# Kernel tuning notes

Measured on AMD Instinct MI355X. Metric: run time of the kernel, lower is better.

Reference implementation:

```python
import jax, jax.numpy as jnp
import numpy as np

B, T, C, H = 2, 2048, 1024, 16
D = C // H  # head_dim = 64

def setup_inputs() -> dict:
    key = jax.random.key(0)
    k1, k2, k3, k4, k5 = jax.random.split(key, 5)
    x = jax.random.normal(k1, (B, T, C), dtype=jnp.float32)
    # RoPE tables (realistic frequencies)
    inv_freq = 1.0 / (10000.0 ** (jnp.arange(0, D // 2, dtype=jnp.float32) / (D // 2)))
    pos = jnp.arange(T, dtype=jnp.float32)
    ang = pos[:, None] * inv_freq[None, :]          # (T, D/2)
    cos, sin = jnp.cos(ang), jnp.sin(ang)
    # causal mask (True = keep)
    mask = jnp.tril(jnp.ones((T, T), dtype=bool))
    W_qkv = jax.random.normal(k2, (3 * C, C), dtype=jnp.float32) * (1.0 / np.sqrt(C))
    W_out = jax.random.normal(k3, (C, C), dtype=jnp.float32) * (1.0 / np.sqrt(C))
    return {"x": x, "cos": cos, "sin": sin, "mask": mask, "W_qkv": W_qkv, "W_out": W_out}

def apply_rope(x, cos, sin):
    # x: (B, H, T, D); cos/sin: (T, D/2)
    d = x.shape[-1] // 2
    x1, x2 = x[..., :d], x[..., d:]
    c = cos[None, None, :x.shape[2], :]
    s = sin[None, None, :x.shape[2], :]
    return jnp.concatenate([x1 * c - x2 * s, x2 * c + x1 * s], axis=-1)

def reference(x, cos, sin, mask, W_qkv, W_out):
    b, t, c = x.shape
    qkv = (x @ W_qkv.T).reshape(b, t, 3, H, D)
    q, k, v = qkv[:, :, 0], qkv[:, :, 1], qkv[:, :, 2]   # (b, t, H, D)
    q = q.transpose(0, 2, 1, 3)
    k = k.transpose(0, 2, 1, 3)
    v = v.transpose(0, 2, 1, 3)                           # (b, H, t, D)
    q = apply_rope(q, cos, sin)
    k = apply_rope(k, cos, sin)
    attn = jnp.einsum('bhqd,bhkd->bhqk', q, k) / jnp.sqrt(jnp.asarray(D, x.dtype))
    attn = jnp.where(mask[None, None, :, :], attn, -jnp.inf)
    attn = jax.nn.softmax(attn, axis=-1)
    out = jnp.einsum('bhqk,bhkd->bhqd', attn, v)          # (b, H, t, D)
    out = out.transpose(0, 2, 1, 3).reshape(b, t, c)
    return out @ W_out.T
```

## Files before the change

kernel.cpp:

```cpp
#include <hip/hip_runtime.h>
#include <stdint.h>

typedef __bf16 bf16;
typedef __bf16 bf16x4 __attribute__((ext_vector_type(4)));
typedef __bf16 bf16x8 __attribute__((ext_vector_type(8)));
typedef float f32x4 __attribute__((ext_vector_type(4)));

#define TSEQ 2048
#define NHEAD 16
#define HDIM 64
#define CDIM 1024

#define AS1(p) ((const __attribute__((address_space(1))) void*)(p))
#define AS3(p) ((__attribute__((address_space(3))) void*)(p))

#if __has_builtin(__builtin_amdgcn_exp2f)
#define EXP2(x) __builtin_amdgcn_exp2f(x)
#else
#define EXP2(x) exp2f(x)
#endif

__global__ __launch_bounds__(256) void cast3_bf16(const float* __restrict__ in1, int n1,
                                                  const float* __restrict__ in2, int n2,
                                                  const float* __restrict__ in3, int n3,
                                                  bf16* __restrict__ out1,
                                                  bf16* __restrict__ out2,
                                                  bf16* __restrict__ out3) {
  int i = (blockIdx.x * 256 + threadIdx.x) * 8;
  const float* src;
  bf16* dst;
  if (i < n1) {
    src = in1 + i; dst = out1 + i;
  } else if (i < n1 + n2) {
    src = in2 + (i - n1); dst = out2 + (i - n1);
  } else if (i < n1 + n2 + n3) {
    src = in3 + (i - n1 - n2); dst = out3 + (i - n1 - n2);
  } else {
    return;
  }
  float4 a = *(const float4*)src;
  float4 b = *(const float4*)(src + 4);
  bf16x8 r;
  r[0] = (bf16)a.x; r[1] = (bf16)a.y; r[2] = (bf16)a.z; r[3] = (bf16)a.w;
  r[4] = (bf16)b.x; r[5] = (bf16)b.y; r[6] = (bf16)b.z; r[7] = (bf16)b.w;
  *(bf16x8*)dst = r;
}

__global__ __launch_bounds__(256) void gemm_qkv_rope(const bf16* __restrict__ A,
                                                     const bf16* __restrict__ B,
                                                     const float* __restrict__ cosb,
                                                     const float* __restrict__ sinb,
                                                     bf16* __restrict__ Qb,
                                                     bf16* __restrict__ Kb,
                                                     bf16* __restrict__ Vt) {
  constexpr int K = 1024;
  __shared__ bf16 smem[8704];
  const int t = threadIdx.x;
  const int w = t >> 6, l = t & 63, g = l >> 4, ln = l & 15;
  const int wm = (w >> 1) * 64, wn = (w & 1) * 64;
  const int m0 = blockIdx.x * 128, n0 = blockIdx.y * 128;
  const int r0 = t >> 2, kc0 = (t & 3) * 8;

  f32x4 acc[4][4] = {};

  for (int k0 = 0; k0 < K; k0 += 32) {
    __syncthreads();
    __builtin_amdgcn_global_load_lds(AS1(A + (size_t)(m0 + r0) * K + k0 + kc0),
                                     AS3(&smem[t * 8]), 16, 0, 0);
    __builtin_amdgcn_global_load_lds(AS1(A + (size_t)(m0 + r0 + 64) * K + k0 + kc0),
                                     AS3(&smem[(t + 256) * 8]), 16, 0, 0);
    __builtin_amdgcn_global_load_lds(AS1(B + (size_t)(n0 + r0) * K + k0 + kc0),
                                     AS3(&smem[4096 + t * 8]), 16, 0, 0);
    __builtin_amdgcn_global_load_lds(AS1(B + (size_t)(n0 + r0 + 64) * K + k0 + kc0),
                                     AS3(&smem[4096 + (t + 256) * 8]), 16, 0, 0);
    __syncthreads();
    bf16x8 af[4], bfr[4];
#pragma unroll
    for (int i = 0; i < 4; i++) {
      af[i] = *(const bf16x8*)&smem[(wm + i * 16 + ln) * 32 + g * 8];
      bfr[i] = *(const bf16x8*)&smem[4096 + (wn + i * 16 + ln) * 32 + g * 8];
    }
#pragma unroll
    for (int i = 0; i < 4; i++)
#pragma unroll
      for (int j = 0; j < 4; j++)
        acc[i][j] = __builtin_amdgcn_mfma_f32_16x16x32_bf16(af[i], bfr[j], acc[i][j], 0, 0, 0);
  }

  const int part = n0 >> 10;
  if (part < 2) {
    bf16* dst = part ? Kb : Qb;
    const float qs = part ? 1.0f : 0.18033688011112042f;
#pragma unroll
    for (int i = 0; i < 4; i++)
#pragma unroll
      for (int j = 0; j < 2; j++) {
        int nl = (n0 & 1023) + wn + j * 16 + ln;
        int h = nl >> 6, d = nl & 31;
#pragma unroll
        for (int r = 0; r < 4; r++) {
          int row = m0 + wm + i * 16 + g * 4 + r;
          int tok = row & (TSEQ - 1), bb = row >> 11;
          float c = cosb[tok * 32 + d], s = sinb[tok * 32 + d];
          float a1 = acc[i][j][r], a2 = acc[i][j + 2][r];
          size_t ob = ((size_t)(bb * NHEAD + h) * TSEQ + tok) * HDIM + d;
          dst[ob] = (bf16)((a1 * c - a2 * s) * qs);
          dst[ob + 32] = (bf16)((a2 * c + a1 * s) * qs);
        }
      }
  } else {
    const int bb = m0 >> 11;
    const int tbase = m0 & (TSEQ - 1);
    const int nbase = n0 - 2048;
#pragma unroll
    for (int pass = 0; pass < 2; pass++) {
      __syncthreads();
      if ((w >> 1) == pass) {
#pragma unroll
        for (int i = 0; i < 4; i++)
#pragma unroll
          for (int j = 0; j < 4; j++) {
            int lr = i * 16 + g * 4;
            int lc = wn + j * 16 + ln;
#pragma unroll
            for (int r = 0; r < 4; r++)
              smem[(lr + r) * 132 + lc] = (bf16)acc[i][j][r];
          }
      }
      __syncthreads();
      for (int c = t; c < 1024; c += 256) {
        int ch = c >> 3, tc = c & 7;
        bf16x8 o;
#pragma unroll
        for (int j2 = 0; j2 < 8; j2++) o[j2] = smem[(tc * 8 + j2) * 132 + ch];
        int n = nbase + ch;
        int h = n >> 6, d = n & 63;
        *(bf16x8*)(Vt + ((size_t)((bb * NHEAD + h) * HDIM + d)) * TSEQ +
                   tbase + pass * 64 + tc * 8) = o;
      }
    }
  }
}

__global__ __launch_bounds__(256) void gemm_out(const bf16* __restrict__ A,
                                                const bf16* __restrict__ B,
                                                float* __restrict__ C,
                                                int M, int N, int K) {
  __shared__ bf16 smem[8192];
  const int t = threadIdx.x;
  const int w = t >> 6, l = t & 63, g = l >> 4, ln = l & 15;
  const int wm = (w >> 1) * 64, wn = (w & 1) * 64;
  const int m0 = blockIdx.x * 128, n0 = blockIdx.y * 128;
  const int r0 = t >> 2, kc0 = (t & 3) * 8;

  f32x4 acc[4][4] = {};

  for (int k0 = 0; k0 < K; k0 += 32) {
    __syncthreads();
    __builtin_amdgcn_global_load_lds(AS1(A + (size_t)(m0 + r0) * K + k0 + kc0),
                                     AS3(&smem[t * 8]), 16, 0, 0);
    __builtin_amdgcn_global_load_lds(AS1(A + (size_t)(m0 + r0 + 64) * K + k0 + kc0),
                                     AS3(&smem[(t + 256) * 8]), 16, 0, 0);
    __builtin_amdgcn_global_load_lds(AS1(B + (size_t)(n0 + r0) * K + k0 + kc0),
                                     AS3(&smem[4096 + t * 8]), 16, 0, 0);
    __builtin_amdgcn_global_load_lds(AS1(B + (size_t)(n0 + r0 + 64) * K + k0 + kc0),
                                     AS3(&smem[4096 + (t + 256) * 8]), 16, 0, 0);
    __syncthreads();
    bf16x8 af[4], bfr[4];
#pragma unroll
    for (int i = 0; i < 4; i++) {
      af[i] = *(const bf16x8*)&smem[(wm + i * 16 + ln) * 32 + g * 8];
      bfr[i] = *(const bf16x8*)&smem[4096 + (wn + i * 16 + ln) * 32 + g * 8];
    }
#pragma unroll
    for (int i = 0; i < 4; i++)
#pragma unroll
      for (int j = 0; j < 4; j++)
        acc[i][j] = __builtin_amdgcn_mfma_f32_16x16x32_bf16(af[i], bfr[j], acc[i][j], 0, 0, 0);
  }
#pragma unroll
  for (int i = 0; i < 4; i++)
#pragma unroll
    for (int j = 0; j < 4; j++) {
      int row = m0 + wm + i * 16 + g * 4;
      int col = n0 + wn + j * 16 + ln;
#pragma unroll
      for (int r = 0; r < 4; r++)
        C[(size_t)(row + r) * N + col] = acc[i][j][r];
    }
}

__global__ __launch_bounds__(1024, 4) void attn_fwd(const bf16* __restrict__ Q,
                                                    const bf16* __restrict__ K,
                                                    const bf16* __restrict__ Vt,
                                                    bf16* __restrict__ ctx) {
  __shared__ __align__(16) char smem_raw[65536];
  bf16* Ks = (bf16*)smem_raw;
  bf16* VTs = (bf16*)(smem_raw + 16384);
  bf16* Ps = (bf16*)(smem_raw + 32768);
  float* Mbuf = (float*)smem_raw;
  float* Lbuf = (float*)(smem_raw + 32768);

  const int t = threadIdx.x;
  const int w = t >> 6;
  const int p = w >> 3;
  const int wq = w & 7;
  const int l = t & 63, g = l >> 4, ln = l & 15;
  const int bid = blockIdx.x;
  const int bh = bid & 31;
  const int qb0 = 15 - (bid >> 5);
  const size_t base = (size_t)bh * TSEQ * HDIM;

  const int q0 = qb0 * 128;
  const int qwb = q0 + wq * 16;
  const int dtile = qwb >> 6;
  const int q_g = qwb + ln;
  const int lswz = (ln & 7) * 8;

  const int ts = t >> 9;
  const int tt = t & 511;
  const int r0 = tt >> 3, ch0 = (tt & 7) * 8;
  const int sidx = r0 * 64 + (((tt & 7) ^ (r0 & 7)) * 8);

  bf16x8 bq[2];
  bq[0] = *(const bf16x8*)(Q + base + (size_t)q_g * HDIM + g * 8);
  bq[1] = *(const bf16x8*)(Q + base + (size_t)q_g * HDIM + 32 + g * 8);

  const bf16* kp = K + base + (size_t)(ts * 64 + r0) * HDIM + ch0;
  const bf16* vp = Vt + base + (size_t)r0 * TSEQ + ts * 64 + ch0;
  bf16x8 kr = *(const bf16x8*)kp;
  bf16x8 vr = *(const bf16x8*)vp;

  f32x4 acc[4] = {};
  float l_run = 0.f;

  for (int i = 0; i <= qb0; i++) {
    __syncthreads();
    *(bf16x8*)&Ks[ts * 4096 + sidx] = kr;
    *(bf16x8*)&VTs[ts * 4096 + sidx] = vr;
    __syncthreads();
    if (i < qb0) {
      kr = *(const bf16x8*)(kp + (size_t)(i + 1) * 128 * HDIM);
      vr = *(const bf16x8*)(vp + (i + 1) * 128);
    }
    const int kt = 2 * i + p;
    if (kt <= dtile) {
      f32x4 st[4] = {};
      __builtin_amdgcn_s_setprio(1);
#pragma unroll
      for (int step = 0; step < 2; step++)
#pragma unroll
        for (int mt = 0; mt < 4; mt++) {
          bf16x8 ak = *(const bf16x8*)&Ks[p * 4096 + (mt * 16 + ln) * 64 +
                                          ((step * 32 + g * 8) ^ lswz)];
          st[mt] = __builtin_amdgcn_mfma_f32_16x16x32_bf16(ak, bq[step], st[mt], 0, 0, 0);
        }
      __builtin_amdgcn_s_setprio(0);
      float vals[16];
      if (kt == dtile) {
#pragma unroll
        for (int mt = 0; mt < 4; mt++)
#pragma unroll
          for (int r = 0; r < 4; r++) {
            int kg = kt * 64 + mt * 16 + g * 4 + r;
            vals[mt * 4 + r] = (kg <= q_g) ? st[mt][r] : -INFINITY;
          }
      } else {
#pragma unroll
        for (int mt = 0; mt < 4; mt++)
#pragma unroll
          for (int r = 0; r < 4; r++) vals[mt * 4 + r] = st[mt][r];
      }
      float psum = 0.f;
#pragma unroll
      for (int i2 = 0; i2 < 16; i2++) {
        float pv = EXP2(vals[i2]);
        vals[i2] = pv;
        psum += pv;
      }
      psum += __shfl_xor(psum, 16);
      psum += __shfl_xor(psum, 32);
      l_run += psum;
#pragma unroll
      for (int mt = 0; mt < 4; mt++) {
        bf16x4 pk;
#pragma unroll
        for (int r = 0; r < 4; r++) pk[r] = (bf16)vals[mt * 4 + r];
        *(bf16x4*)&Ps[w * 1024 + ln * 64 +
                      (((mt * 16 + (g >> 1) * 8) ^ lswz) + (g & 1) * 4)] = pk;
      }
      __builtin_amdgcn_s_setprio(1);
#pragma unroll
      for (int step = 0; step < 2; step++) {
        bf16x8 ap = *(const bf16x8*)&Ps[w * 1024 + ln * 64 + ((step * 32 + g * 8) ^ lswz)];
#pragma unroll
        for (int nt = 0; nt < 4; nt++) {
          bf16x8 bv = *(const bf16x8*)&VTs[p * 4096 + (nt * 16 + ln) * 64 +
                                           ((step * 32 + g * 8) ^ lswz)];
          acc[nt] = __builtin_amdgcn_mfma_f32_16x16x32_bf16(ap, bv, acc[nt], 0, 0, 0);
        }
      }
      __builtin_amdgcn_s_setprio(0);
    }
  }

  __syncthreads();
  if (p == 1) {
#pragma unroll
    for (int nt = 0; nt < 4; nt++)
      *(f32x4*)&Mbuf[(wq * 64 + l) * 16 + nt * 4] = acc[nt];
    Lbuf[wq * 64 + l] = l_run;
  }
  __syncthreads();
  if (p == 0) {
#pragma unroll
    for (int nt = 0; nt < 4; nt++) acc[nt] += *(const f32x4*)&Mbuf[(wq * 64 + l) * 16 + nt * 4];
    l_run += Lbuf[wq * 64 + l];
    float inv = 1.0f / l_run;
    float lrow[4];
#pragma unroll
    for (int r = 0; r < 4; r++) lrow[r] = __shfl(inv, g * 4 + r, 64);
    const int b = bh >> 4, h = bh & (NHEAD - 1);
#pragma unroll
    for (int nt = 0; nt < 4; nt++)
#pragma unroll
      for (int r = 0; r < 4; r++) {
        int q = qwb + g * 4 + r;
        ctx[(size_t)(b * TSEQ + q) * CDIM + h * HDIM + nt * 16 + ln] =
            (bf16)(acc[nt][r] * lrow[r]);
      }
  }
}

extern "C" void kernel_launch(void* const* d_in, const int* in_sizes, int n_in,
                              void* d_out, int out_size, void* d_ws, size_t ws_size,
                              hipStream_t stream) {
  const float* x = (const float*)d_in[0];
  const float* cosb = (const float*)d_in[1];
  const float* sinb = (const float*)d_in[2];
  const float* Wqkv = (const float*)d_in[4];
  const float* Wout = (const float*)d_in[5];
  float* out = (float*)d_out;

  char* ws = (char*)d_ws;
  bf16* x_bf = (bf16*)ws;
  bf16* ctx = (bf16*)ws;
  bf16* Wqkv_bf = (bf16*)(ws + 8388608);
  bf16* Wout_bf = (bf16*)(ws + 14680064);
  bf16* Qb = (bf16*)(ws + 16777216);
  bf16* Kb = (bf16*)(ws + 25165824);
  bf16* Vt = (bf16*)(ws + 33554432);

  cast3_bf16<<<(4194304 + 3145728 + 1048576) / 8 / 256, 256, 0, stream>>>(
      x, 4194304, Wqkv, 3145728, Wout, 1048576, x_bf, Wqkv_bf, Wout_bf);
  gemm_qkv_rope<<<dim3(32, 24), 256, 0, stream>>>(x_bf, Wqkv_bf, cosb, sinb, Qb, Kb, Vt);
  attn_fwd<<<512, 1024, 0, stream>>>(Qb, Kb, Vt, ctx);
  gemm_out<<<dim3(32, 8), 256, 0, stream>>>(ctx, Wout_bf, out, 4096, 1024, 1024);
}
```

Measured before the change: 184.3 us.

## Triple-buffer LDS in QKV GEMM with async global-to-LDS prefetch

```diff
diff --git a/kernel.cpp b/kernel.cpp
--- a/kernel.cpp
+++ b/kernel.cpp
@@ -54,7 +54,121 @@
                                                      bf16* __restrict__ Kb,
                                                      bf16* __restrict__ Vt) {
   constexpr int K = 1024;
-  __shared__ bf16 smem[8704];
+  __shared__ bf16 smem[24576];
+  const int t = threadIdx.x;
+  const int w = t >> 6, l = t & 63, g = l >> 4, ln = l & 15;
+  const int wm = (w >> 1) * 64, wn = (w & 1) * 64;
+  const int m0 = blockIdx.x * 128, n0 = blockIdx.y * 128;
+  const int r0 = t >> 2, kc0 = (t & 3) * 8;
+
+  f32x4 acc[4][4] = {};
+
+#define STAGE_G1(buf, k0)                                                             \
+  do {                                                                                \
+    __builtin_amdgcn_global_load_lds(AS1(A + (size_t)(m0 + r0) * K + (k0) + kc0),     \
+                                     AS3(&smem[(buf) * 8192 + t * 8]), 16, 0, 0);     \
+    __builtin_amdgcn_global_load_lds(AS1(A + (size_t)(m0 + r0 + 64) * K + (k0) + kc0),\
+                                     AS3(&smem[(buf) * 8192 + (t + 256) * 8]), 16, 0, 0); \
+    __builtin_amdgcn_global_load_lds(AS1(B + (size_t)(n0 + r0) * K + (k0) + kc0),     \
+                                     AS3(&smem[(buf) * 8192 + 4096 + t * 8]), 16, 0, 0);  \
+    __builtin_amdgcn_global_load_lds(AS1(B + (size_t)(n0 + r0 + 64) * K + (k0) + kc0),\
+                                     AS3(&smem[(buf) * 8192 + 4096 + (t + 256) * 8]), 16, 0, 0); \
+  } while (0)
+
+  STAGE_G1(0, 0);
+  STAGE_G1(1, 32);
+  asm volatile("s_waitcnt vmcnt(4) lgkmcnt(0)" ::: "memory");
+  __builtin_amdgcn_s_barrier();
+  asm volatile("" ::: "memory");
+
+  for (int it = 0; it < 32; ++it) {
+    const int cur = it % 3;
+    if (it < 30) STAGE_G1((it + 2) % 3, (it + 2) * 32);
+    const bf16* sa = &smem[cur * 8192];
+    const bf16* sb = &smem[cur * 8192 + 4096];
+    bf16x8 af[4], bfr[4];
+#pragma unroll
+    for (int i = 0; i < 4; i++) {
+      af[i] = *(const bf16x8*)&sa[(wm + i * 16 + ln) * 32 + g * 8];
+      bfr[i] = *(const bf16x8*)&sb[(wn + i * 16 + ln) * 32 + g * 8];
+    }
+#pragma unroll
+    for (int i = 0; i < 4; i++)
+#pragma unroll
+      for (int j = 0; j < 4; j++)
+        acc[i][j] = __builtin_amdgcn_mfma_f32_16x16x32_bf16(af[i], bfr[j], acc[i][j], 0, 0, 0);
+    if (it < 30) {
+      asm volatile("s_waitcnt vmcnt(4) lgkmcnt(0)" ::: "memory");
+      __builtin_amdgcn_s_barrier();
+      asm volatile("" ::: "memory");
+    } else if (it == 30) {
+      asm volatile("s_waitcnt vmcnt(0) lgkmcnt(0)" ::: "memory");
+      __builtin_amdgcn_s_barrier();
+      asm volatile("" ::: "memory");
+    }
+  }
+#undef STAGE_G1
+
+  const int part = n0 >> 10;
+  if (part < 2) {
+    bf16* dst = part ? Kb : Qb;
+    const float qs = part ? 1.0f : 0.18033688011112042f;
+#pragma unroll
+    for (int i = 0; i < 4; i++)
+#pragma unroll
+      for (int j = 0; j < 2; j++) {
+        int nl = (n0 & 1023) + wn + j * 16 + ln;
+        int h = nl >> 6, d = nl & 31;
+#pragma unroll
+        for (int r = 0; r < 4; r++) {
+          int row = m0 + wm + i * 16 + g * 4 + r;
+          int tok = row & (TSEQ - 1), bb = row >> 11;
+          float c = cosb[tok * 32 + d], s = sinb[tok * 32 + d];
+          float a1 = acc[i][j][r], a2 = acc[i][j + 2][r];
+          size_t ob = ((size_t)(bb * NHEAD + h) * TSEQ + tok) * HDIM + d;
+          dst[ob] = (bf16)((a1 * c - a2 * s) * qs);
+          dst[ob + 32] = (bf16)((a2 * c + a1 * s) * qs);
+        }
+      }
+  } else {
+    const int bb = m0 >> 11;
+    const int tbase = m0 & (TSEQ - 1);
+    const int nbase = n0 - 2048;
+#pragma unroll
+    for (int pass = 0; pass < 2; pass++) {
+      __syncthreads();
+      if ((w >> 1) == pass) {
+#pragma unroll
+        for (int i = 0; i < 4; i++)
+#pragma unroll
+          for (int j = 0; j < 4; j++) {
+            int lr = i * 16 + g * 4;
+            int lc = wn + j * 16 + ln;
+#pragma unroll
+            for (int r = 0; r < 4; r++)
+              smem[(lr + r) * 132 + lc] = (bf16)acc[i][j][r];
+          }
+      }
+      __syncthreads();
+      for (int c = t; c < 1024; c += 256) {
+        int ch = c >> 3, tc = c & 7;
+        bf16x8 o;
+#pragma unroll
+        for (int j2 = 0; j2 < 8; j2++) o[j2] = smem[(tc * 8 + j2) * 132 + ch];
+        int n = nbase + ch;
+        int h = n >> 6, d = n & 63;
+        *(bf16x8*)(Vt + ((size_t)((bb * NHEAD + h) * HDIM + d)) * TSEQ +
+                   tbase + pass * 64 + tc * 8) = o;
+      }
+    }
+  }
+}
+
+__global__ __launch_bounds__(256) void gemm_out(const bf16* __restrict__ A,
+                                                const bf16* __restrict__ B,
+                                                float* __restrict__ C,
+                                                int M, int N, int K) {
+  __shared__ bf16 smem[8192];
   const int t = threadIdx.x;
   const int w = t >> 6, l = t & 63, g = l >> 4, ln = l & 15;
   const int wm = (w >> 1) * 64, wn = (w & 1) * 64;
@@ -86,98 +200,6 @@
       for (int j = 0; j < 4; j++)
         acc[i][j] = __builtin_amdgcn_mfma_f32_16x16x32_bf16(af[i], bfr[j], acc[i][j], 0, 0, 0);
   }
-
-  const int part = n0 >> 10;
-  if (part < 2) {
-    bf16* dst = part ? Kb : Qb;
-    const float qs = part ? 1.0f : 0.18033688011112042f;
-#pragma unroll
-    for (int i = 0; i < 4; i++)
-#pragma unroll
-      for (int j = 0; j < 2; j++) {
-        int nl = (n0 & 1023) + wn + j * 16 + ln;
-        int h = nl >> 6, d = nl & 31;
-#pragma unroll
-        for (int r = 0; r < 4; r++) {
-          int row = m0 + wm + i * 16 + g * 4 + r;
-          int tok = row & (TSEQ - 1), bb = row >> 11;
-          float c = cosb[tok * 32 + d], s = sinb[tok * 32 + d];
-          float a1 = acc[i][j][r], a2 = acc[i][j + 2][r];
-          size_t ob = ((size_t)(bb * NHEAD + h) * TSEQ + tok) * HDIM + d;
-          dst[ob] = (bf16)((a1 * c - a2 * s) * qs);
-          dst[ob + 32] = (bf16)((a2 * c + a1 * s) * qs);
-        }
-      }
-  } else {
-    const int bb = m0 >> 11;
-    const int tbase = m0 & (TSEQ - 1);
-    const int nbase = n0 - 2048;
-#pragma unroll
-    for (int pass = 0; pass < 2; pass++) {
-      __syncthreads();
-      if ((w >> 1) == pass) {
-#pragma unroll
-        for (int i = 0; i < 4; i++)
-#pragma unroll
-          for (int j = 0; j < 4; j++) {
-            int lr = i * 16 + g * 4;
-            int lc = wn + j * 16 + ln;
-#pragma unroll
-            for (int r = 0; r < 4; r++)
-              smem[(lr + r) * 132 + lc] = (bf16)acc[i][j][r];
-          }
-      }
-      __syncthreads();
-      for (int c = t; c < 1024; c += 256) {
-        int ch = c >> 3, tc = c & 7;
-        bf16x8 o;
-#pragma unroll
-        for (int j2 = 0; j2 < 8; j2++) o[j2] = smem[(tc * 8 + j2) * 132 + ch];
-        int n = nbase + ch;
-        int h = n >> 6, d = n & 63;
-        *(bf16x8*)(Vt + ((size_t)((bb * NHEAD + h) * HDIM + d)) * TSEQ +
-                   tbase + pass * 64 + tc * 8) = o;
-      }
-    }
-  }
-}
-
-__global__ __launch_bounds__(256) void gemm_out(const bf16* __restrict__ A,
-                                                const bf16* __restrict__ B,
-                                                float* __restrict__ C,
-                                                int M, int N, int K) {
-  __shared__ bf16 smem[8192];
-  const int t = threadIdx.x;
-  const int w = t >> 6, l = t & 63, g = l >> 4, ln = l & 15;
-  const int wm = (w >> 1) * 64, wn = (w & 1) * 64;
-  const int m0 = blockIdx.x * 128, n0 = blockIdx.y * 128;
-  const int r0 = t >> 2, kc0 = (t & 3) * 8;
-
-  f32x4 acc[4][4] = {};
-
-  for (int k0 = 0; k0 < K; k0 += 32) {
-    __syncthreads();
-    __builtin_amdgcn_global_load_lds(AS1(A + (size_t)(m0 + r0) * K + k0 + kc0),
-                                     AS3(&smem[t * 8]), 16, 0, 0);
-    __builtin_amdgcn_global_load_lds(AS1(A + (size_t)(m0 + r0 + 64) * K + k0 + kc0),
-                                     AS3(&smem[(t + 256) * 8]), 16, 0, 0);
-    __builtin_amdgcn_global_load_lds(AS1(B + (size_t)(n0 + r0) * K + k0 + kc0),
-                                     AS3(&smem[4096 + t * 8]), 16, 0, 0);
-    __builtin_amdgcn_global_load_lds(AS1(B + (size_t)(n0 + r0 + 64) * K + k0 + kc0),
-                                     AS3(&smem[4096 + (t + 256) * 8]), 16, 0, 0);
-    __syncthreads();
-    bf16x8 af[4], bfr[4];
-#pragma unroll
-    for (int i = 0; i < 4; i++) {
-      af[i] = *(const bf16x8*)&smem[(wm + i * 16 + ln) * 32 + g * 8];
-      bfr[i] = *(const bf16x8*)&smem[4096 + (wn + i * 16 + ln) * 32 + g * 8];
-    }
-#pragma unroll
-    for (int i = 0; i < 4; i++)
-#pragma unroll
-      for (int j = 0; j < 4; j++)
-        acc[i][j] = __builtin_amdgcn_mfma_f32_16x16x32_bf16(af[i], bfr[j], acc[i][j], 0, 0, 0);
-  }
 #pragma unroll
   for (int i = 0; i < 4; i++)
 #pragma unroll
```

Result: no change. 185.3 us (+0.5%).
